# Kernel optimization log

Measured on AMD Instinct MI355X. Metric: run time of the kernel, lower is better.

## Reference

```python
import jax, jax.numpy as jnp
import numpy as np

N_QUBITS = 3
N_LAYERS = 2
EPS = 1e-12  # torch F.normalize eps


def _apply_1q(state, U, q):
    # state: (B, 2, 2, 2) complex, qubit q on axis q+1 (wire 0 = MSB, PennyLane convention)
    ax = q + 1
    s = jnp.moveaxis(state, ax, -1)
    s = jnp.einsum('...j,ij->...i', s, U)
    return jnp.moveaxis(s, -1, ax)


def _apply_cnot(state, c, t):
    # flip target qubit t where control qubit c is |1>
    ca, ta = c + 1, t + 1
    s0 = jnp.take(state, 0, axis=ca)
    s1 = jnp.take(state, 1, axis=ca)
    flip_ax = ta if ta < ca else ta - 1  # axis index after removing ca
    s1 = jnp.flip(s1, axis=flip_ax)
    return jnp.stack([s0, s1], axis=ca)


def _ry(theta):
    c, s = jnp.cos(theta / 2), jnp.sin(theta / 2)
    return jnp.array([[c, -s], [s, c]]).astype(jnp.complex64)


def _rz(theta):
    return jnp.array([[jnp.exp(-1j * theta / 2), 0.0 + 0.0j],
                      [0.0 + 0.0j, jnp.exp(1j * theta / 2)]]).astype(jnp.complex64)


def setup_inputs() -> dict:
    key = jax.random.key(0)
    k1, k2, k3, k4 = jax.random.split(key, 4)
    B, F, V = 262144, 512, 8
    x = jax.random.normal(k1, (B, F), dtype=jnp.float32)
    # nn.Linear(512, 8): kaiming-uniform-ish init
    bound = 1.0 / np.sqrt(F)
    W_proj = jax.random.uniform(k2, (V, F), minval=-bound, maxval=bound, dtype=jnp.float32)
    b_proj = jax.random.uniform(k3, (V,), minval=-bound, maxval=bound, dtype=jnp.float32)
    # TorchLayer default init: uniform in [0, 2pi); shape (n_layers, 2, n_qubits)
    vqc_weights = jax.random.uniform(k4, (N_LAYERS, 2, N_QUBITS), minval=0.0,
                                     maxval=2 * np.pi, dtype=jnp.float32)
    return {"x": x, "W_proj": W_proj, "b_proj": b_proj, "vqc_weights": vqc_weights}


def reference(x, W_proj, b_proj, vqc_weights):
    B = x.shape[0]
    projected = jnp.tanh(x @ W_proj.T + b_proj)                       # (B, 8)
    norm = jnp.linalg.norm(projected, axis=1, keepdims=True)
    projected_norm = projected / jnp.maximum(norm, EPS)               # (B, 8), unit L2
    # AmplitudeEmbedding(normalize=True): state amplitudes = normalized vector
    state = projected_norm.astype(jnp.complex64).reshape(B, 2, 2, 2)  # wire0 = MSB
    for l in range(N_LAYERS):
        for q in range(N_QUBITS):
            state = _apply_1q(state, _ry(vqc_weights[l, 0, q]), q)
        for q in range(N_QUBITS):
            state = _apply_1q(state, _rz(vqc_weights[l, 1, q]), q)
        for q in range(N_QUBITS - 1):
            state = _apply_cnot(state, q, q + 1)
        state = _apply_cnot(state, N_QUBITS - 1, 0)
    probs = state.real ** 2 + state.imag ** 2                         # (B, 2, 2, 2)
    z = []
    for q in range(N_QUBITS):
        p = jnp.moveaxis(probs, q + 1, 1).reshape(B, 2, -1)
        z.append(p[:, 0].sum(-1) - p[:, 1].sum(-1))                   # <Z_q>
    quantum_out = jnp.stack(z, axis=1)                                # (B, 3)
    return jnp.concatenate([projected, quantum_out], axis=1)          # (B, 11)
```

## Files before the change

### kernel.cpp

```cpp
#include <hip/hip_runtime.h>
#include <math.h>

__global__ __launch_bounds__(64) void vqc_build_u(const float* __restrict__ wq,
                                                  float* __restrict__ Uws) {
  const int j = threadIdx.x;
  if (j >= 8) return;
  float ar[8], ai[8];
#pragma unroll
  for (int i = 0; i < 8; ++i) { ar[i] = (i == j) ? 1.f : 0.f; ai[i] = 0.f; }

#pragma unroll
  for (int l = 0; l < 2; ++l) {
#pragma unroll
    for (int q = 0; q < 3; ++q) {
      const float th = 0.5f * wq[l * 6 + q];
      const float c = cosf(th), s = sinf(th);
      const int bit = 4 >> q;
#pragma unroll
      for (int i0 = 0; i0 < 8; ++i0) {
        if (i0 & bit) continue;
        const int i1 = i0 | bit;
        const float r0 = ar[i0], m0 = ai[i0], r1 = ar[i1], m1 = ai[i1];
        ar[i0] = c * r0 - s * r1;  ai[i0] = c * m0 - s * m1;
        ar[i1] = s * r0 + c * r1;  ai[i1] = s * m0 + c * m1;
      }
    }
#pragma unroll
    for (int q = 0; q < 3; ++q) {
      const float th = 0.5f * wq[l * 6 + 3 + q];
      const float c = cosf(th), s = sinf(th);
      const int bit = 4 >> q;
#pragma unroll
      for (int i = 0; i < 8; ++i) {
        const float r = ar[i], m = ai[i];
        if (i & bit) { ar[i] = r * c - m * s;  ai[i] = m * c + r * s; }
        else         { ar[i] = r * c + m * s;  ai[i] = m * c - r * s; }
      }
    }
#pragma unroll
    for (int k = 0; k < 3; ++k) {
      const int cb = (k == 0) ? 4 : (k == 1) ? 2 : 1;
      const int tb = (k == 0) ? 2 : (k == 1) ? 1 : 4;
#pragma unroll
      for (int i = 0; i < 8; ++i) {
        if ((i & cb) && !(i & tb)) {
          const int i1 = i | tb;
          float t;
          t = ar[i]; ar[i] = ar[i1]; ar[i1] = t;
          t = ai[i]; ai[i] = ai[i1]; ai[i1] = t;
        }
      }
    }
  }
#pragma unroll
  for (int i = 0; i < 8; ++i) {
    Uws[i * 8 + j]      = ar[i];
    Uws[64 + i * 8 + j] = ai[i];
  }
}

template<bool GUARD>
__global__ __launch_bounds__(256, 2) void vqc_fused(const float* __restrict__ x,
                                                    const float* __restrict__ W,
                                                    const float* __restrict__ bias,
                                                    const float* __restrict__ Uws,
                                                    float* __restrict__ out, int B) {
  const int lane = threadIdx.x & 63;
  const int wid  = blockIdx.x * (blockDim.x >> 6) + (threadIdx.x >> 6);
  const int nw   = gridDim.x * (blockDim.x >> 6);
  const bool b0 = (lane & 1) != 0;
  const bool b1 = (lane & 2) != 0;
  const bool b2 = (lane & 4) != 0;
  const int grp = lane >> 3;
  const int myv = ((lane & 1) << 2) | (lane & 2) | ((lane >> 2) & 1);

  float w0[8][4], w1[8][4];
#pragma unroll
  for (int v = 0; v < 8; ++v) {
    const float4 a = *(const float4*)(W + v * 512 + lane * 4);
    const float4 b = *(const float4*)(W + v * 512 + 256 + lane * 4);
    w0[v][0] = a.x; w0[v][1] = a.y; w0[v][2] = a.z; w0[v][3] = a.w;
    w1[v][0] = b.x; w1[v][1] = b.y; w1[v][2] = b.z; w1[v][3] = b.w;
  }
  float Ur[8], Ui[8];
#pragma unroll
  for (int i = 0; i < 8; ++i) {
    Ur[i] = Uws[i * 8 + myv];
    Ui[i] = Uws[64 + i * 8 + myv];
  }
  const float bv = bias[myv];

  const int nbatch = (B + 7) >> 3;
  for (int rb = wid; rb < nbatch; rb += nw) {
    const size_t r0 = (size_t)rb << 3;

    float4 xa[8], xb[8];
#pragma unroll
    for (int t = 0; t < 8; ++t) {
      size_t r = r0 + t;
      if (GUARD) r = (r < (size_t)B) ? r : (size_t)(B - 1);
      const float4* xr = (const float4*)(x + r * 512);
      xa[t] = xr[lane];
      xb[t] = xr[64 + lane];
    }

    float myd = 0.f;
#pragma unroll
    for (int t = 0; t < 8; ++t) {
      float acc[8];
#pragma unroll
      for (int v = 0; v < 8; ++v) {
        float s = xa[t].x * w0[v][0];
        s = fmaf(xa[t].y, w0[v][1], s);
        s = fmaf(xa[t].z, w0[v][2], s);
        s = fmaf(xa[t].w, w0[v][3], s);
        s = fmaf(xb[t].x, w1[v][0], s);
        s = fmaf(xb[t].y, w1[v][1], s);
        s = fmaf(xb[t].z, w1[v][2], s);
        s = fmaf(xb[t].w, w1[v][3], s);
        acc[v] = s;
      }
      float s4[4];
#pragma unroll
      for (int i = 0; i < 4; ++i) {
        const float keep = b0 ? acc[i + 4] : acc[i];
        const float send = b0 ? acc[i] : acc[i + 4];
        s4[i] = keep + __shfl_xor(send, 1, 64);
      }
      float s2[2];
#pragma unroll
      for (int i = 0; i < 2; ++i) {
        const float keep = b1 ? s4[i + 2] : s4[i];
        const float send = b1 ? s4[i] : s4[i + 2];
        s2[i] = keep + __shfl_xor(send, 2, 64);
      }
      const float keep = b2 ? s2[1] : s2[0];
      const float send = b2 ? s2[0] : s2[1];
      float s1 = keep + __shfl_xor(send, 4, 64);
      s1 += __shfl_xor(s1, 8, 64);
      s1 += __shfl_xor(s1, 16, 64);
      s1 += __shfl_xor(s1, 32, 64);
      myd = (grp == t) ? s1 : myd;
    }

    const size_t row = r0 + grp;
    const float p = tanhf(myd + bv);
    float ss = p * p;
    ss += __shfl_xor(ss, 1, 64);
    ss += __shfl_xor(ss, 2, 64);
    ss += __shfl_xor(ss, 4, 64);
    const float av = p * (1.0f / fmaxf(sqrtf(ss), 1e-12f));

    float q[16];
#pragma unroll
    for (int i = 0; i < 8; ++i) {
      q[2 * i]     = Ur[i] * av;
      q[2 * i + 1] = Ui[i] * av;
    }
    float n8[8];
#pragma unroll
    for (int i = 0; i < 8; ++i) {
      const float k1 = b0 ? q[i + 8] : q[i];
      const float s1v = b0 ? q[i] : q[i + 8];
      n8[i] = k1 + __shfl_xor(s1v, 1, 64);
    }
    float n4[4];
#pragma unroll
    for (int i = 0; i < 4; ++i) {
      const float k2 = b1 ? n8[i + 4] : n8[i];
      const float s2v = b1 ? n8[i] : n8[i + 4];
      n4[i] = k2 + __shfl_xor(s2v, 2, 64);
    }
    float n2[2];
#pragma unroll
    for (int i = 0; i < 2; ++i) {
      const float k3 = b2 ? n4[i + 2] : n4[i];
      const float s3v = b2 ? n4[i] : n4[i + 2];
      n2[i] = k3 + __shfl_xor(s3v, 4, 64);
    }
    const float pr = n2[0] * n2[0] + n2[1] * n2[1];
    float t0 = (myv & 4) ? -pr : pr;
    float t1 = (myv & 2) ? -pr : pr;
    float t2 = (myv & 1) ? -pr : pr;
#pragma unroll
    for (int m = 1; m <= 4; m <<= 1) {
      t0 += __shfl_xor(t0, m, 64);
      t1 += __shfl_xor(t1, m, 64);
      t2 += __shfl_xor(t2, m, 64);
    }
    if (!GUARD || row < (size_t)B) {
      float* o = out + row * 11;
      o[myv] = p;
      if (myv < 3) o[8 + myv] = (myv == 0) ? t0 : ((myv == 1) ? t1 : t2);
    }
  }
}

extern "C" void kernel_launch(void* const* d_in, const int* in_sizes, int n_in,
                              void* d_out, int out_size, void* d_ws, size_t ws_size,
                              hipStream_t stream) {
  const float* x  = (const float*)d_in[0];
  const float* W  = (const float*)d_in[1];
  const float* b  = (const float*)d_in[2];
  const float* wq = (const float*)d_in[3];
  float* out = (float*)d_out;
  float* Uws = (float*)d_ws;

  const int B = in_sizes[0] / 512;

  vqc_build_u<<<1, 64, 0, stream>>>(wq, Uws);
  if (B & 7)
    vqc_fused<true><<<2048, 256, 0, stream>>>(x, W, b, Uws, out, B);
  else
    vqc_fused<false><<<2048, 256, 0, stream>>>(x, W, b, Uws, out, B);
}
```

Measured before the change: 114.9 us.

## Fuse unitary build into main kernel, use nontemporal x loads, size grid to work

Removes the separate single-block kernel that builds the 8x8 circuit unitary and has each lane compute its own unitary column inline, which saves one launch and its dependency. Loads of x become nontemporal to avoid polluting cache with streaming data. The grid becomes one wave per 8-row batch instead of a fixed 2048-block persistent grid. Every wave now redoes the trig and gate work and reloads W, which adds per-wave setup cost now that waves no longer loop over many batches.

```diff
diff --git a/kernel.cpp b/kernel.cpp
--- a/kernel.cpp
+++ b/kernel.cpp
@@ -1,69 +1,13 @@
 #include <hip/hip_runtime.h>
 #include <math.h>
 
-__global__ __launch_bounds__(64) void vqc_build_u(const float* __restrict__ wq,
-                                                  float* __restrict__ Uws) {
-  const int j = threadIdx.x;
-  if (j >= 8) return;
-  float ar[8], ai[8];
-#pragma unroll
-  for (int i = 0; i < 8; ++i) { ar[i] = (i == j) ? 1.f : 0.f; ai[i] = 0.f; }
-
-#pragma unroll
-  for (int l = 0; l < 2; ++l) {
-#pragma unroll
-    for (int q = 0; q < 3; ++q) {
-      const float th = 0.5f * wq[l * 6 + q];
-      const float c = cosf(th), s = sinf(th);
-      const int bit = 4 >> q;
-#pragma unroll
-      for (int i0 = 0; i0 < 8; ++i0) {
-        if (i0 & bit) continue;
-        const int i1 = i0 | bit;
-        const float r0 = ar[i0], m0 = ai[i0], r1 = ar[i1], m1 = ai[i1];
-        ar[i0] = c * r0 - s * r1;  ai[i0] = c * m0 - s * m1;
-        ar[i1] = s * r0 + c * r1;  ai[i1] = s * m0 + c * m1;
-      }
-    }
-#pragma unroll
-    for (int q = 0; q < 3; ++q) {
-      const float th = 0.5f * wq[l * 6 + 3 + q];
-      const float c = cosf(th), s = sinf(th);
-      const int bit = 4 >> q;
-#pragma unroll
-      for (int i = 0; i < 8; ++i) {
-        const float r = ar[i], m = ai[i];
-        if (i & bit) { ar[i] = r * c - m * s;  ai[i] = m * c + r * s; }
-        else         { ar[i] = r * c + m * s;  ai[i] = m * c - r * s; }
-      }
-    }
-#pragma unroll
-    for (int k = 0; k < 3; ++k) {
-      const int cb = (k == 0) ? 4 : (k == 1) ? 2 : 1;
-      const int tb = (k == 0) ? 2 : (k == 1) ? 1 : 4;
-#pragma unroll
-      for (int i = 0; i < 8; ++i) {
-        if ((i & cb) && !(i & tb)) {
-          const int i1 = i | tb;
-          float t;
-          t = ar[i]; ar[i] = ar[i1]; ar[i1] = t;
-          t = ai[i]; ai[i] = ai[i1]; ai[i1] = t;
-        }
-      }
-    }
-  }
-#pragma unroll
-  for (int i = 0; i < 8; ++i) {
-    Uws[i * 8 + j]      = ar[i];
-    Uws[64 + i * 8 + j] = ai[i];
-  }
-}
+typedef float f32x4 __attribute__((ext_vector_type(4)));
 
 template<bool GUARD>
 __global__ __launch_bounds__(256, 2) void vqc_fused(const float* __restrict__ x,
                                                     const float* __restrict__ W,
                                                     const float* __restrict__ bias,
-                                                    const float* __restrict__ Uws,
+                                                    const float* __restrict__ wq,
                                                     float* __restrict__ out, int B) {
   const int lane = threadIdx.x & 63;
   const int wid  = blockIdx.x * (blockDim.x >> 6) + (threadIdx.x >> 6);
@@ -77,31 +21,72 @@
   float w0[8][4], w1[8][4];
 #pragma unroll
   for (int v = 0; v < 8; ++v) {
-    const float4 a = *(const float4*)(W + v * 512 + lane * 4);
-    const float4 b = *(const float4*)(W + v * 512 + 256 + lane * 4);
+    const f32x4 a = *(const f32x4*)(W + v * 512 + lane * 4);
+    const f32x4 b = *(const f32x4*)(W + v * 512 + 256 + lane * 4);
     w0[v][0] = a.x; w0[v][1] = a.y; w0[v][2] = a.z; w0[v][3] = a.w;
     w1[v][0] = b.x; w1[v][1] = b.y; w1[v][2] = b.z; w1[v][3] = b.w;
   }
+  const float bv = bias[myv];
+
   float Ur[8], Ui[8];
 #pragma unroll
-  for (int i = 0; i < 8; ++i) {
-    Ur[i] = Uws[i * 8 + myv];
-    Ui[i] = Uws[64 + i * 8 + myv];
+  for (int i = 0; i < 8; ++i) { Ur[i] = (i == myv) ? 1.f : 0.f; Ui[i] = 0.f; }
+#pragma unroll
+  for (int l = 0; l < 2; ++l) {
+#pragma unroll
+    for (int q = 0; q < 3; ++q) {
+      const float th = 0.5f * wq[l * 6 + q];
+      const float c = cosf(th), s = sinf(th);
+      const int bit = 4 >> q;
+#pragma unroll
+      for (int i0 = 0; i0 < 8; ++i0) {
+        if (i0 & bit) continue;
+        const int i1 = i0 | bit;
+        const float r0 = Ur[i0], m0 = Ui[i0], r1 = Ur[i1], m1 = Ui[i1];
+        Ur[i0] = c * r0 - s * r1;  Ui[i0] = c * m0 - s * m1;
+        Ur[i1] = s * r0 + c * r1;  Ui[i1] = s * m0 + c * m1;
+      }
+    }
+#pragma unroll
+    for (int q = 0; q < 3; ++q) {
+      const float th = 0.5f * wq[l * 6 + 3 + q];
+      const float c = cosf(th), s = sinf(th);
+      const int bit = 4 >> q;
+#pragma unroll
+      for (int i = 0; i < 8; ++i) {
+        const float r = Ur[i], m = Ui[i];
+        if (i & bit) { Ur[i] = r * c - m * s;  Ui[i] = m * c + r * s; }
+        else         { Ur[i] = r * c + m * s;  Ui[i] = m * c - r * s; }
+      }
+    }
+#pragma unroll
+    for (int k = 0; k < 3; ++k) {
+      const int cb = (k == 0) ? 4 : (k == 1) ? 2 : 1;
+      const int tb = (k == 0) ? 2 : (k == 1) ? 1 : 4;
+#pragma unroll
+      for (int i = 0; i < 8; ++i) {
+        if ((i & cb) && !(i & tb)) {
+          const int i1 = i | tb;
+          float t;
+          t = Ur[i]; Ur[i] = Ur[i1]; Ur[i1] = t;
+          t = Ui[i]; Ui[i] = Ui[i1]; Ui[i1] = t;
+        }
+      }
+    }
   }
-  const float bv = bias[myv];
 
   const int nbatch = (B + 7) >> 3;
   for (int rb = wid; rb < nbatch; rb += nw) {
     const size_t r0 = (size_t)rb << 3;
 
-    float4 xa[8], xb[8];
+    f32x4 xa[8], xb[8];
 #pragma unroll
     for (int t = 0; t < 8; ++t) {
       size_t r = r0 + t;
       if (GUARD) r = (r < (size_t)B) ? r : (size_t)(B - 1);
-      const float4* xr = (const float4*)(x + r * 512);
-      xa[t] = xr[lane];
-      xb[t] = xr[64 + lane];
+      const f32x4* xr = (const f32x4*)(x + r * 512);
+      xa[t] = __builtin_nontemporal_load(&xr[lane]);
+      xb[t] = __builtin_nontemporal_load(&xr[64 + lane]);
     }
 
     float myd = 0.f;
@@ -204,13 +189,15 @@
   const float* b  = (const float*)d_in[2];
   const float* wq = (const float*)d_in[3];
   float* out = (float*)d_out;
-  float* Uws = (float*)d_ws;
 
   const int B = in_sizes[0] / 512;
-
-  vqc_build_u<<<1, 64, 0, stream>>>(wq, Uws);
+  const int nbatch = (B + 7) >> 3;
+  const int waves_needed = nbatch;
+  int blocks = (waves_needed + 3) >> 2;
+  if (blocks > 65535 * 16) blocks = 65535 * 16;
+
   if (B & 7)
-    vqc_fused<true><<<2048, 256, 0, stream>>>(x, W, b, Uws, out, B);
+    vqc_fused<true><<<blocks, 256, 0, stream>>>(x, W, b, wq, out, B);
   else
-    vqc_fused<false><<<2048, 256, 0, stream>>>(x, W, b, Uws, out, B);
+    vqc_fused<false><<<blocks, 256, 0, stream>>>(x, W, b, wq, out, B);
 }
```

After: 119.2 us. 1.04x slower.
